# Performance work log

Measured on AMD Instinct MI355X. Metric: run time of the kernel, lower is better.

## Reference

```python
import jax, jax.numpy as jnp
import numpy as np

B, P, D = 8, 1024, 1024
H, N = 16, 64  # num_heads, head_dim


def setup_inputs() -> dict:
    key = jax.random.key(0)
    k1, k2, k3 = jax.random.split(key, 3)
    inputs = jax.random.normal(k1, (B, P, D), dtype=jnp.float32)
    # Keras 'random_normal' initializer: stddev 0.05
    w_qkv = jax.random.normal(k2, (H, 3, D, N), dtype=jnp.float32) * 0.05
    w_o = jax.random.normal(k3, (N * H, D), dtype=jnp.float32) * 0.05
    return {"inputs": inputs, "w_qkv": w_qkv, "w_o": w_o}


def reference(inputs, w_qkv, w_o):
    # Per-head QKV projection: [b,p,d] x [h,3,d,n] -> [b,h,3,p,n]
    proj = jnp.einsum('bpv,havn->bhapn', inputs, w_qkv)
    q = proj[:, :, 0]  # [b,h,p,n]
    k = proj[:, :, 1]
    v = proj[:, :, 2]
    head_dim = q.shape[-1]
    scale = 1.0 / jnp.sqrt(jnp.asarray(head_dim, dtype=jnp.float32))
    scores = jnp.einsum('bhqn,bhkn->bhqk', q, k) * scale  # [b,h,p,p]
    attn = jax.nn.softmax(scores, axis=-1)
    out = jnp.einsum('bhqk,bhkn->bhqn', attn, v)  # [b,h,p,n]
    # concat heads along feature dim: [b,p,h*n]
    b, h, p, n = out.shape
    concat = out.transpose(0, 2, 1, 3).reshape(b, p, h * n)
    return jnp.einsum('bpi,ij->bpj', concat, w_o)  # [b,p,d_model]
```

## Files before the change

### kernel.cpp

```cpp
#include <hip/hip_runtime.h>
#include <stdint.h>

typedef _Float16 f16;
typedef __attribute__((ext_vector_type(4))) _Float16 f16x4;
typedef __attribute__((ext_vector_type(8))) _Float16 f16x8;
typedef __attribute__((ext_vector_type(4))) float f32x4;

__device__ __forceinline__ void gload_lds16(const void* g, void* l) {
  __builtin_amdgcn_global_load_lds(
      (__attribute__((address_space(1))) void*)const_cast<void*>(g),
      (__attribute__((address_space(3))) void*)l, 16, 0, 0);
}


__global__ void convert_x(const float* __restrict__ in, f16* __restrict__ out) {
  int i = blockIdx.x * 256 + threadIdx.x;
  float4 v = ((const float4*)in)[i];
  f16x4 hv;
  hv[0] = (f16)v.x; hv[1] = (f16)v.y; hv[2] = (f16)v.z; hv[3] = (f16)v.w;
  ((f16x4*)out)[i] = hv;
}

__global__ void transpose_wqkv(const float* __restrict__ in, f16* __restrict__ out) {
  __shared__ float tile[64][65];
  int s = blockIdx.x >> 4;
  int vt = blockIdx.x & 15;
  int hh = s / 3, a = s - hh * 3;
  int tx = threadIdx.x & 63, ty = threadIdx.x >> 6;
#pragma unroll
  for (int i = 0; i < 16; i++) {
    int r = i * 4 + ty;
    tile[r][tx] = in[((size_t)(s * 1024 + vt * 64 + r)) * 64 + tx];
  }
  __syncthreads();
#pragma unroll
  for (int i = 0; i < 16; i++) {
    int n = i * 4 + ty;
    out[((size_t)(a * 1024 + hh * 64 + n)) * 1024 + vt * 64 + tx] = (f16)tile[tx][n];
  }
}

__global__ void transpose_wo(const float* __restrict__ in, f16* __restrict__ out) {
  __shared__ float tile[64][65];
  int rt = blockIdx.x >> 4, ct = blockIdx.x & 15;
  int tx = threadIdx.x & 63, ty = threadIdx.x >> 6;
#pragma unroll
  for (int i = 0; i < 16; i++) {
    int r = i * 4 + ty;
    tile[r][tx] = in[((size_t)(rt * 64 + r)) * 1024 + ct * 64 + tx];
  }
  __syncthreads();
#pragma unroll
  for (int i = 0; i < 16; i++) {
    int j = i * 4 + ty;
    out[((size_t)(ct * 64 + j)) * 1024 + rt * 64 + tx] = (f16)tile[tx][j];
  }
}

template <int OUTMODE>
__global__ __launch_bounds__(256, 2) void gemm_kernel(
    const f16* __restrict__ A, const f16* __restrict__ BT, void* __restrict__ out,
    void* __restrict__ out2, int M, int N, int K) {
  __shared__ __align__(16) f16 As[128][32];
  __shared__ __align__(16) f16 Bs[128][32];
  const int t = threadIdx.x;
  const int lane = t & 63, wave = t >> 6;
  const int lr = lane & 15, lg = lane >> 4;
  const int wm = wave >> 1, wn = wave & 1;
  const int nTN = N >> 7;
  const int bm = blockIdx.x / nTN, bn = blockIdx.x % nTN;
  const f16* Ab = A + (size_t)bm * 128 * K;
  const f16* Bb = BT + (size_t)bn * 128 * K;

  const f32x4 zero4 = {0.f, 0.f, 0.f, 0.f};
  f32x4 acc[4][4];
#pragma unroll
  for (int m = 0; m < 4; m++)
#pragma unroll
    for (int n = 0; n < 4; n++) acc[m][n] = zero4;

  for (int k0 = 0; k0 < K; k0 += 32) {
    __syncthreads();
#pragma unroll
    for (int i = 0; i < 2; i++) {
      int q = wave * 2 + i;
      int e = q * 64 + lane;
      int r = e >> 2, bi = e & 3;
      gload_lds16(Ab + (size_t)r * K + k0 + ((bi ^ (r & 3)) << 3),
                  (char*)&As[0][0] + q * 1024);
      gload_lds16(Bb + (size_t)r * K + k0 + ((bi ^ (r & 3)) << 3),
                  (char*)&Bs[0][0] + q * 1024);
    }
    __syncthreads();
    f16x8 af[4], bf[4];
#pragma unroll
    for (int m = 0; m < 4; m++) {
      int r = wm * 64 + m * 16 + lr;
      af[m] = *(const f16x8*)&As[r][(lg ^ (r & 3)) << 3];
    }
#pragma unroll
    for (int n = 0; n < 4; n++) {
      int r = wn * 64 + n * 16 + lr;
      bf[n] = *(const f16x8*)&Bs[r][(lg ^ (r & 3)) << 3];
    }
#pragma unroll
    for (int m = 0; m < 4; m++)
#pragma unroll
      for (int n = 0; n < 4; n++)
        acc[m][n] = __builtin_amdgcn_mfma_f32_16x16x32_f16(af[m], bf[n], acc[m][n], 0, 0, 0);
  }

  const int r0 = bm * 128 + wm * 64;
  const int c0 = bn * 128 + wn * 64;
  if (OUTMODE == 2 && bn >= 16) {
    f16* VT = (f16*)out2;
    const int bb = bm >> 3;
#pragma unroll
    for (int m = 0; m < 4; m++) {
      int p = r0 + m * 16 + lg * 4;
      int pl = p & 1023;
#pragma unroll
      for (int n = 0; n < 4; n++) {
        int vcol = c0 - 2048 + n * 16 + lr;
        f16x4 pv;
#pragma unroll
        for (int i = 0; i < 4; i++) pv[i] = (f16)acc[m][n][i];
        *(f16x4*)&VT[((size_t)(bb * 16 + (vcol >> 6)) * 64 + (vcol & 63)) * 1024 + pl] = pv;
      }
    }
  } else {
#pragma unroll
    for (int m = 0; m < 4; m++)
#pragma unroll
      for (int n = 0; n < 4; n++)
#pragma unroll
        for (int i = 0; i < 4; i++) {
          int gr = r0 + m * 16 + lg * 4 + i;
          int gc = c0 + n * 16 + lr;
          if (OUTMODE == 1)
            ((float*)out)[(size_t)gr * N + gc] = acc[m][n][i];
          else
            ((f16*)out)[(size_t)gr * N + gc] = (f16)acc[m][n][i];
        }
  }
}

__global__ __launch_bounds__(256, 4) void attn_kernel(
    const f16* __restrict__ QKV, const f16* __restrict__ VT, f16* __restrict__ C) {
  __shared__ __align__(16) f16 smem[16384];

  const int t = threadIdx.x, lane = t & 63, wave = t >> 6;
  const int lr = lane & 15, lg = lane >> 4;
  const int pt = blockIdx.x, bh = blockIdx.y;
  const int b = bh >> 4, h = bh & 15;
  const int p0 = pt * 128;

  const f16* Qg = QKV + ((size_t)(b * 1024 + p0)) * 3072 + h * 64;
  const f16* Kg = QKV + ((size_t)(b * 1024)) * 3072 + 1024 + h * 64;
  const f16* Vg = VT + (size_t)bh * 64 * 1024;

#pragma unroll
  for (int i = 0; i < 4; i++) {
    int q = wave * 4 + i;
    int u = q * 64 + lane;
    int r = u >> 3, j = u & 7;
    gload_lds16(Qg + (size_t)r * 3072 + ((j ^ (r & 7)) << 3), (char*)smem + q * 1024);
  }
  __syncthreads();

  f16x8 qa[2][2];
#pragma unroll
  for (int m = 0; m < 2; m++)
#pragma unroll
    for (int hh = 0; hh < 2; hh++) {
      int r = wave * 32 + m * 16 + lr;
      qa[m][hh] = *(const f16x8*)&smem[(size_t)r * 64 + (((hh * 4 + lg) ^ (lr & 7)) << 3)];
    }
  __syncthreads();

  auto STAGE = [&](int kc, int cur) {
#pragma unroll
    for (int i = 0; i < 2; i++) {
      int q = wave * 2 + i;
      int u = q * 64 + lane;
      int r = u >> 3, j = u & 7;
      gload_lds16(Kg + (size_t)(kc * 64 + r) * 3072 + ((j ^ (r & 7)) << 3),
                  (char*)smem + cur * 16384 + q * 1024);
      gload_lds16(Vg + (size_t)r * 1024 + kc * 64 + ((j ^ (r & 7)) << 3),
                  (char*)smem + cur * 16384 + 8192 + q * 1024);
    }
  };

  STAGE(0, 0);
  STAGE(1, 1);
  __syncthreads();

  const f32x4 zero4 = {0.f, 0.f, 0.f, 0.f};
  f32x4 o[2][4];
#pragma unroll
  for (int m = 0; m < 2; m++)
#pragma unroll
    for (int n = 0; n < 4; n++) o[m][n] = zero4;
  float mrun[2] = {-1e30f, -1e30f};
  float lrun[2] = {0.f, 0.f};

#pragma unroll 1
  for (int kc = 0; kc < 16; kc++) {
    const int cur = kc & 1;
    const int kB = cur * 8192;
    const char* vB = (const char*)smem + cur * 16384 + 8192;

    f32x4 s[2][4];
#pragma unroll
    for (int m = 0; m < 2; m++)
#pragma unroll
      for (int kb = 0; kb < 4; kb++) s[m][kb] = zero4;
    __builtin_amdgcn_s_setprio(1);
#pragma unroll
    for (int kb = 0; kb < 4; kb++) {
      int r = kb * 16 + lr;
      f16x8 kf0 = *(const f16x8*)&smem[kB + (size_t)r * 64 + ((lg ^ (lr & 7)) << 3)];
      f16x8 kf1 = *(const f16x8*)&smem[kB + (size_t)r * 64 + (((4 + lg) ^ (lr & 7)) << 3)];
#pragma unroll
      for (int m = 0; m < 2; m++) {
        s[m][kb] = __builtin_amdgcn_mfma_f32_16x16x32_f16(kf0, qa[m][0], s[m][kb], 0, 0, 0);
        s[m][kb] = __builtin_amdgcn_mfma_f32_16x16x32_f16(kf1, qa[m][1], s[m][kb], 0, 0, 0);
      }
    }
    __builtin_amdgcn_s_setprio(0);

    f16x4 pa[2][4];
#pragma unroll
    for (int m = 0; m < 2; m++) {
      float mx01 = fmaxf(fmaxf(s[m][0][0], s[m][0][1]), fmaxf(s[m][0][2], s[m][0][3]));
      float mx23 = fmaxf(fmaxf(s[m][1][0], s[m][1][1]), fmaxf(s[m][1][2], s[m][1][3]));
      float mx45 = fmaxf(fmaxf(s[m][2][0], s[m][2][1]), fmaxf(s[m][2][2], s[m][2][3]));
      float mx67 = fmaxf(fmaxf(s[m][3][0], s[m][3][1]), fmaxf(s[m][3][2], s[m][3][3]));
      float mx = fmaxf(fmaxf(mx01, mx23), fmaxf(mx45, mx67));
      mx = fmaxf(mx, __shfl_xor(mx, 16));
      mx = fmaxf(mx, __shfl_xor(mx, 32));
      mx *= 0.125f;
      if (__any(mx > mrun[m] + 3.0f)) {
        float mnew = fmaxf(mrun[m], mx);
        float alpha = __expf(mrun[m] - mnew);
        mrun[m] = mnew;
        lrun[m] *= alpha;
#pragma unroll
        for (int i = 0; i < 4; i++) {
          float ai = __shfl(alpha, (lane & 48) | (lg * 4 + i));
#pragma unroll
          for (int n = 0; n < 4; n++) o[m][n][i] *= ai;
        }
      }
      float mt = mrun[m] * 1.44269504f;
      float rs = 0.f;
#pragma unroll
      for (int kb = 0; kb < 4; kb++)
#pragma unroll
        for (int i = 0; i < 4; i++) {
          float p = exp2f(fmaf(s[m][kb][i], 0.180336878f, -mt));
          rs += p;
          pa[m][kb][i] = (f16)p;
        }
      rs += __shfl_xor(rs, 16);
      rs += __shfl_xor(rs, 32);
      lrun[m] += rs;
    }

    __builtin_amdgcn_s_setprio(1);
#pragma unroll
    for (int n = 0; n < 4; n++) {
#pragma unroll
      for (int kb = 0; kb < 4; kb++) {
        const f16x4 vb = *(const f16x4*)(vB + (size_t)(n * 16 + lr) * 128 +
                                         ((((kb * 2 + (lg >> 1)) ^ (lr & 7)) << 4) | ((lg & 1) << 3)));
        o[0][n] = __builtin_amdgcn_mfma_f32_16x16x16f16(pa[0][kb], vb, o[0][n], 0, 0, 0);
        o[1][n] = __builtin_amdgcn_mfma_f32_16x16x16f16(pa[1][kb], vb, o[1][n], 0, 0, 0);
      }
    }
    __builtin_amdgcn_s_setprio(0);

    __syncthreads();
    if (kc + 2 < 16) STAGE(kc + 2, cur);
  }

#pragma unroll
  for (int m = 0; m < 2; m++) {
    float linv = 1.f / lrun[m];
#pragma unroll
    for (int i = 0; i < 4; i++) {
      float li = __shfl(linv, (lane & 48) | (lg * 4 + i));
      int prow = p0 + wave * 32 + m * 16 + lg * 4 + i;
#pragma unroll
      for (int n = 0; n < 4; n++) {
        int col = h * 64 + n * 16 + lr;
        C[((size_t)(b * 1024 + prow)) * 1024 + col] = (f16)(o[m][n][i] * li);
      }
    }
  }
}

extern "C" void kernel_launch(void* const* d_in, const int* in_sizes, int n_in,
                              void* d_out, int out_size, void* d_ws, size_t ws_size,
                              hipStream_t stream) {
  const float* X = (const float*)d_in[0];
  const float* Wqkv = (const float*)d_in[1];
  const float* Wo = (const float*)d_in[2];
  float* Y = (float*)d_out;

  f16* ws = (f16*)d_ws;
  f16* X16 = ws;
  f16* WqkvT = ws + 8388608;
  f16* WoT = ws + 11534336;
  f16* QKV = ws + 12582912;
  f16* VT = (f16*)d_out;

  convert_x<<<8192, 256, 0, stream>>>(X, X16);
  transpose_wqkv<<<768, 256, 0, stream>>>(Wqkv, WqkvT);
  transpose_wo<<<256, 256, 0, stream>>>(Wo, WoT);
  gemm_kernel<2><<<64 * 24, 256, 0, stream>>>(X16, WqkvT, QKV, VT, 8192, 3072, 1024);
  attn_kernel<<<dim3(8, 128), 256, 0, stream>>>(QKV, VT, X16 );
  gemm_kernel<1><<<64 * 8, 256, 0, stream>>>(X16 , WoT, Y, nullptr, 8192, 1024, 1024);
}
```

Baseline: 192.0 us.

## Fold softmax scale into Q and max-offset into MFMA accumulator; use 16x16x32 PV MFMA

Pre-scales Q by scale*log2e in fp16 so the scores come out in the log2 domain, and seeds the QK accumulator with -mrun so the exp2 needs no FMA. The lazy rescale now uses a threshold in log2 units. P is packed with cvt_pkrtz, row sums are taken with fdot2, and the PV product switches from 16x16x16 to 16x16x32 MFMA by pairing K blocks. This trims VALU work in the softmax and halves the PV MFMA count. In exchange, Q is rounded in fp16 after scaling and P uses round-toward-zero, which slightly changes precision.

```diff
diff --git a/kernel.cpp b/kernel.cpp
--- a/kernel.cpp
+++ b/kernel.cpp
@@ -2,8 +2,10 @@
 #include <stdint.h>
 
 typedef _Float16 f16;
+typedef __attribute__((ext_vector_type(2))) _Float16 f16x2;
 typedef __attribute__((ext_vector_type(4))) _Float16 f16x4;
 typedef __attribute__((ext_vector_type(8))) _Float16 f16x8;
+typedef __attribute__((ext_vector_type(2))) __fp16 h16x2;
 typedef __attribute__((ext_vector_type(4))) float f32x4;
 
 __device__ __forceinline__ void gload_lds16(const void* g, void* l) {
@@ -168,13 +170,17 @@
   }
   __syncthreads();
 
+  const f16 qscale = (f16)0.180336878f;
   f16x8 qa[2][2];
 #pragma unroll
   for (int m = 0; m < 2; m++)
 #pragma unroll
     for (int hh = 0; hh < 2; hh++) {
       int r = wave * 32 + m * 16 + lr;
-      qa[m][hh] = *(const f16x8*)&smem[(size_t)r * 64 + (((hh * 4 + lg) ^ (lr & 7)) << 3)];
+      f16x8 v = *(const f16x8*)&smem[(size_t)r * 64 + (((hh * 4 + lg) ^ (lr & 7)) << 3)];
+#pragma unroll
+      for (int e = 0; e < 8; e++) v[e] *= qscale;
+      qa[m][hh] = v;
     }
   __syncthreads();
 
@@ -201,8 +207,9 @@
   for (int m = 0; m < 2; m++)
 #pragma unroll
     for (int n = 0; n < 4; n++) o[m][n] = zero4;
-  float mrun[2] = {-1e30f, -1e30f};
+  float mrun[2] = {0.f, 0.f};
   float lrun[2] = {0.f, 0.f};
+  const h16x2 one2 = {(__fp16)1.f, (__fp16)1.f};
 
 #pragma unroll 1
   for (int kc = 0; kc < 16; kc++) {
@@ -212,9 +219,11 @@
 
     f32x4 s[2][4];
 #pragma unroll
-    for (int m = 0; m < 2; m++)
-#pragma unroll
-      for (int kb = 0; kb < 4; kb++) s[m][kb] = zero4;
+    for (int m = 0; m < 2; m++) {
+      f32x4 init = {-mrun[m], -mrun[m], -mrun[m], -mrun[m]};
+#pragma unroll
+      for (int kb = 0; kb < 4; kb++) s[m][kb] = init;
+    }
     __builtin_amdgcn_s_setprio(1);
 #pragma unroll
     for (int kb = 0; kb < 4; kb++) {
@@ -229,22 +238,24 @@
     }
     __builtin_amdgcn_s_setprio(0);
 
-    f16x4 pa[2][4];
+    f16x8 pa8[2][2];
 #pragma unroll
     for (int m = 0; m < 2; m++) {
-      float mx01 = fmaxf(fmaxf(s[m][0][0], s[m][0][1]), fmaxf(s[m][0][2], s[m][0][3]));
-      float mx23 = fmaxf(fmaxf(s[m][1][0], s[m][1][1]), fmaxf(s[m][1][2], s[m][1][3]));
-      float mx45 = fmaxf(fmaxf(s[m][2][0], s[m][2][1]), fmaxf(s[m][2][2], s[m][2][3]));
-      float mx67 = fmaxf(fmaxf(s[m][3][0], s[m][3][1]), fmaxf(s[m][3][2], s[m][3][3]));
-      float mx = fmaxf(fmaxf(mx01, mx23), fmaxf(mx45, mx67));
+      float mx = fmaxf(fmaxf(fmaxf(s[m][0][0], s[m][0][1]), fmaxf(s[m][0][2], s[m][0][3])),
+                       fmaxf(fmaxf(s[m][1][0], s[m][1][1]), fmaxf(s[m][1][2], s[m][1][3])));
+      mx = fmaxf(mx, fmaxf(fmaxf(fmaxf(s[m][2][0], s[m][2][1]), fmaxf(s[m][2][2], s[m][2][3])),
+                           fmaxf(fmaxf(s[m][3][0], s[m][3][1]), fmaxf(s[m][3][2], s[m][3][3]))));
       mx = fmaxf(mx, __shfl_xor(mx, 16));
       mx = fmaxf(mx, __shfl_xor(mx, 32));
-      mx *= 0.125f;
-      if (__any(mx > mrun[m] + 3.0f)) {
-        float mnew = fmaxf(mrun[m], mx);
-        float alpha = __expf(mrun[m] - mnew);
-        mrun[m] = mnew;
+      if (__any(mx > 4.328085f)) {
+        float delta = fmaxf(mx, 0.f);
+        mrun[m] += delta;
+        float alpha = exp2f(-delta);
         lrun[m] *= alpha;
+#pragma unroll
+        for (int kb = 0; kb < 4; kb++)
+#pragma unroll
+          for (int i = 0; i < 4; i++) s[m][kb][i] -= delta;
 #pragma unroll
         for (int i = 0; i < 4; i++) {
           float ai = __shfl(alpha, (lane & 48) | (lg * 4 + i));
@@ -252,15 +263,20 @@
           for (int n = 0; n < 4; n++) o[m][n][i] *= ai;
         }
       }
-      float mt = mrun[m] * 1.44269504f;
       float rs = 0.f;
 #pragma unroll
-      for (int kb = 0; kb < 4; kb++)
-#pragma unroll
-        for (int i = 0; i < 4; i++) {
-          float p = exp2f(fmaf(s[m][kb][i], 0.180336878f, -mt));
-          rs += p;
-          pa[m][kb][i] = (f16)p;
+      for (int j = 0; j < 2; j++)
+#pragma unroll
+        for (int hb = 0; hb < 2; hb++) {
+          int kb = 2 * j + hb;
+          h16x2 h01 = __builtin_amdgcn_cvt_pkrtz(exp2f(s[m][kb][0]), exp2f(s[m][kb][1]));
+          h16x2 h23 = __builtin_amdgcn_cvt_pkrtz(exp2f(s[m][kb][2]), exp2f(s[m][kb][3]));
+          rs = __builtin_amdgcn_fdot2(h01, one2, rs, false);
+          rs = __builtin_amdgcn_fdot2(h23, one2, rs, false);
+          pa8[m][j][hb * 4 + 0] = (f16)h01[0];
+          pa8[m][j][hb * 4 + 1] = (f16)h01[1];
+          pa8[m][j][hb * 4 + 2] = (f16)h23[0];
+          pa8[m][j][hb * 4 + 3] = (f16)h23[1];
         }
       rs += __shfl_xor(rs, 16);
       rs += __shfl_xor(rs, 32);
@@ -270,12 +286,14 @@
     __builtin_amdgcn_s_setprio(1);
 #pragma unroll
     for (int n = 0; n < 4; n++) {
-#pragma unroll
-      for (int kb = 0; kb < 4; kb++) {
-        const f16x4 vb = *(const f16x4*)(vB + (size_t)(n * 16 + lr) * 128 +
-                                         ((((kb * 2 + (lg >> 1)) ^ (lr & 7)) << 4) | ((lg & 1) << 3)));
-        o[0][n] = __builtin_amdgcn_mfma_f32_16x16x16f16(pa[0][kb], vb, o[0][n], 0, 0, 0);
-        o[1][n] = __builtin_amdgcn_mfma_f32_16x16x16f16(pa[1][kb], vb, o[1][n], 0, 0, 0);
+      const char* rowB = vB + (size_t)(n * 16 + lr) * 128 + ((lg & 1) << 3);
+#pragma unroll
+      for (int j = 0; j < 2; j++) {
+        f16x4 lo = *(const f16x4*)(rowB + (((j * 4 + (lg >> 1)) ^ (lr & 7)) << 4));
+        f16x4 hi = *(const f16x4*)(rowB + (((j * 4 + 2 + (lg >> 1)) ^ (lr & 7)) << 4));
+        f16x8 vb = {lo[0], lo[1], lo[2], lo[3], hi[0], hi[1], hi[2], hi[3]};
+        o[0][n] = __builtin_amdgcn_mfma_f32_16x16x32_f16(pa8[0][j], vb, o[0][n], 0, 0, 0);
+        o[1][n] = __builtin_amdgcn_mfma_f32_16x16x32_f16(pa8[1][j], vb, o[1][n], 0, 0, 0);
       }
     }
     __builtin_amdgcn_s_setprio(0);
```

Result: no change. 189.5 us (-1.3%).
